# Performance work log

Hardware: AMD Instinct MI355X
Metric: run time of the kernel (lower is better)

## Reference

```python
import jax, jax.numpy as jnp
import numpy as np

NEG = -1e9


def setup_inputs() -> dict:
    key = jax.random.key(0)
    ks = jax.random.split(key, 5)
    B, N, D = 2, 1024, 40
    x = jax.random.normal(ks[0], (B, N, D), dtype=jnp.float32)
    # Linear(2D->D): store as (2D, D) so y = cat @ W1 + b1 (transposed torch layout)
    W1 = jax.random.normal(ks[1], (2 * D, D), dtype=jnp.float32) * (1.0 / np.sqrt(2 * D))
    b1 = jax.random.normal(ks[2], (D,), dtype=jnp.float32) * 0.01
    W2 = jax.random.normal(ks[3], (D, D), dtype=jnp.float32) * (1.0 / np.sqrt(D))
    b2 = jax.random.normal(ks[4], (D,), dtype=jnp.float32) * 0.01
    return {"x": x, "W1": W1, "b1": b1, "W2": W2, "b2": b2}


def reference(x, W1, b1, W2, b2):
    B, N, D = x.shape
    # cat([xi, xj]) @ W1 == xi @ W1[:D] + xj @ W1[D:] -> avoid (B,N,N,2D) materialization
    ai = x @ W1[:D]          # (B, N, D), contribution of row index i
    aj = x @ W1[D:]          # (B, N, D), contribution of col index j
    h = jax.nn.gelu(ai[:, :, None, :] + aj[:, None, :, :] + b1, approximate=False)  # (B,N,N,D)
    p = h @ W2 + b2          # (B, N, N, D)
    mask = jnp.triu(jnp.ones((N, N), dtype=bool), 1)  # True where j > i (masked out)
    p = jnp.where(mask[None, :, :, None], 0.0, p)
    sq = jnp.sum(p * p, axis=-1)                       # (B, N, N)
    s = jnp.sqrt(jnp.where(mask[None], 1.0, sq))       # safe sqrt at masked zeros
    s = jnp.where(mask[None], NEG, s)
    w = jax.nn.softmax(s, axis=-1)                     # softmax over j
    return jnp.sum(w[..., None] * p, axis=2)           # (B, N, D)
```

## Files before the change

### kernel.cpp

```cpp
#include <hip/hip_runtime.h>
#include <math.h>

#define D 40
#define NN 1024
#define BB 2

typedef __attribute__((ext_vector_type(8))) _Float16 f16x8;
typedef __attribute__((ext_vector_type(4))) float f32x4;
typedef __attribute__((ext_vector_type(2))) float f32x2;

__device__ __forceinline__ unsigned int pk16(float a, float b) {
    return __builtin_bit_cast(unsigned int, __builtin_amdgcn_cvt_pkrtz(a, b));
}

__device__ __forceinline__ f32x2 lo2(float4 v) { return (f32x2){v.x, v.y}; }
__device__ __forceinline__ f32x2 hi2(float4 v) { return (f32x2){v.z, v.w}; }

__device__ __forceinline__ unsigned int gelu2pk(f32x2 s) {
    f32x2 u = s * s;
    f32x2 t1 = u * 0.10294366f + 2.3022083f;
    f32x2 z = s * t1;
    f32x2 e = { __builtin_amdgcn_exp2f(z.x), __builtin_amdgcn_exp2f(z.y) };
    e = e + 1.0f;
    f32x2 r = { __builtin_amdgcn_rcpf(e.x), __builtin_amdgcn_rcpf(e.y) };
    f32x2 g = s - s * r;
    return pk16(g.x, g.y);
}

__device__ __forceinline__ void pinf(float& x) { asm volatile("" : "+v"(x)); }
__device__ __forceinline__ void pin4(float4& v) {
    asm volatile("" : "+v"(v.x), "+v"(v.y), "+v"(v.z), "+v"(v.w));
}
__device__ __forceinline__ void pin8(f16x8& v) {
    uint4 u = __builtin_bit_cast(uint4, v);
    asm volatile("" : "+v"(u.x), "+v"(u.y), "+v"(u.z), "+v"(u.w));
    v = __builtin_bit_cast(f16x8, u);
}
__device__ __forceinline__ void pinv4(f32x4& v) {
    asm volatile("" : "+v"(v.x), "+v"(v.y), "+v"(v.z), "+v"(v.w));
}

__device__ __forceinline__ f16x8 frag8(float4 a0, float4 a1, float4 x0, float4 x1) {
    uint4 Bu;
    Bu.x = gelu2pk(lo2(a0) + lo2(x0));
    Bu.y = gelu2pk(hi2(a0) + hi2(x0));
    Bu.z = gelu2pk(lo2(a1) + lo2(x1));
    Bu.w = gelu2pk(hi2(a1) + hi2(x1));
    return __builtin_bit_cast(f16x8, Bu);
}

__global__ __launch_bounds__(256) void precompute_kernel(
    const float* __restrict__ x, const float* __restrict__ W1,
    const float* __restrict__ b1, const float* __restrict__ W2,
    float* __restrict__ ai, float* __restrict__ aj, uint4* __restrict__ w2fT) {
    const int t = threadIdx.x;
    const int bid = blockIdx.x;
    const int r = (bid << 1) + (t >> 7);
    const int tl = t & 127;
    const float* xr = x + (size_t)r * D;

    if (tl < D) {
        const int d = tl;
        float s = b1[d];
#pragma unroll
        for (int k = 0; k < D; ++k) s = fmaf(xr[k], W1[k * D + d], s);
        ai[(size_t)r * D + d] = s;
    } else if (tl >= 64 && tl < 64 + D) {
        const int d = tl - 64;
        float s = 0.0f;
#pragma unroll
        for (int k = 0; k < D; ++k) s = fmaf(xr[k], W1[(D + k) * D + d], s);
        aj[(size_t)r * D + d] = s;
    }

    if (bid == 0 && t < 64) {
        const int lr = t & 15, lg = t >> 4;
#pragma unroll
        for (int mt = 0; mt < 3; ++mt)
#pragma unroll
            for (int kt = 0; kt < 2; ++kt) {
                unsigned int u[4];
#pragma unroll
                for (int pe = 0; pe < 4; ++pe) {
                    int k0 = kt * 32 + lg * 8 + pe * 2;
                    int dd = mt * 16 + lr;
                    float v0 = (k0 < D && dd < D) ? W2[k0 * D + dd] : 0.0f;
                    float v1 = (k0 + 1 < D && dd < D) ? W2[(k0 + 1) * D + dd] : 0.0f;
                    u[pe] = pk16(v0, v1);
                }
                w2fT[(mt * 2 + kt) * 64 + t] = make_uint4(u[0], u[1], u[2], u[3]);
            }
    }
}

__global__ __launch_bounds__(256)
__attribute__((amdgpu_waves_per_eu(4)))
void pair_kernel(
    const float* __restrict__ ai_g, const float* __restrict__ aj_g,
    const uint4* __restrict__ w2fT, const float* __restrict__ b2,
    float* __restrict__ out) {
    __shared__ float mbuf[224];

    const int t = threadIdx.x;
    const int bid = blockIdx.x;
    const int bb = bid & 1;
    const int i = NN - 1 - (bid >> 1);
    const int w = t >> 6;
    const int l = t & 63;
    const int lr = l & 15;
    const int lg = l >> 4;
    const int idxA = lr << 2;

    f16x8 w2t[3][2];
#pragma unroll
    for (int mt = 0; mt < 3; ++mt)
#pragma unroll
        for (int kt = 0; kt < 2; ++kt) {
            w2t[mt][kt] = __builtin_bit_cast(f16x8, w2fT[(mt * 2 + kt) * 64 + l]);
            pin8(w2t[mt][kt]);
        }

    f32x4 bv4[3];
#pragma unroll
    for (int mt = 0; mt < 3; ++mt) {
#pragma unroll
        for (int r = 0; r < 4; ++r) {
            int d = mt * 16 + lg * 4 + r;
            bv4[mt][r] = (d < D) ? b2[d] : 0.0f;
        }
        pinv4(bv4[mt]);
    }

    const float* ai_row = ai_g + ((size_t)bb * NN + i) * D;
    float4 air0 = *reinterpret_cast<const float4*>(ai_row + (lg << 3));
    float4 air1 = *reinterpret_cast<const float4*>(ai_row + (lg << 3) + 4);
    float4 ai32 = *reinterpret_cast<const float4*>(ai_row + 32 + ((l >> 5) << 2));
    pin4(air0); pin4(air1); pin4(ai32);

    const float* aj_b = aj_g + (size_t)bb * NN * D;

    float l_run = 0.0f;
    f32x4 o4[3];
#pragma unroll
    for (int mt = 0; mt < 3; ++mt) o4[mt] = (f32x4){0.0f, 0.0f, 0.0f, 0.0f};

    auto window = [&](int jbase, float4 qa0, float4 qa1, float4 qb0,
                      float4 qb1, float4 qt, bool masked) {
        unsigned int pd0 = gelu2pk(lo2(ai32) + lo2(qt));
        unsigned int pd1 = gelu2pk(hi2(ai32) + hi2(qt));
        uint4 tB0, tB1;
        tB0.x = __builtin_amdgcn_ds_bpermute(idxA,       pd0);
        tB0.y = __builtin_amdgcn_ds_bpermute(idxA,       pd1);
        tB0.z = __builtin_amdgcn_ds_bpermute(idxA + 128, pd0);
        tB0.w = __builtin_amdgcn_ds_bpermute(idxA + 128, pd1);
        tB1.x = __builtin_amdgcn_ds_bpermute(idxA + 64,  pd0);
        tB1.y = __builtin_amdgcn_ds_bpermute(idxA + 64,  pd1);
        tB1.z = __builtin_amdgcn_ds_bpermute(idxA + 192, pd0);
        tB1.w = __builtin_amdgcn_ds_bpermute(idxA + 192, pd1);

        f32x4 acc[3][2];
#pragma unroll
        for (int mt = 0; mt < 3; ++mt)
#pragma unroll
            for (int n = 0; n < 2; ++n)
                acc[mt][n] = bv4[mt];
        {
            f16x8 B = frag8(air0, air1, qa0, qa1);
            f16x8 Bt = __builtin_bit_cast(f16x8, tB0);
#pragma unroll
            for (int mt = 0; mt < 3; ++mt) {
                acc[mt][0] = __builtin_amdgcn_mfma_f32_16x16x32_f16(
                    w2t[mt][0], B, acc[mt][0], 0, 0, 0);
                acc[mt][0] = __builtin_amdgcn_mfma_f32_16x16x32_f16(
                    w2t[mt][1], Bt, acc[mt][0], 0, 0, 0);
            }
        }
        {
            f16x8 B = frag8(air0, air1, qb0, qb1);
            f16x8 Bt = __builtin_bit_cast(f16x8, tB1);
#pragma unroll
            for (int mt = 0; mt < 3; ++mt) {
                acc[mt][1] = __builtin_amdgcn_mfma_f32_16x16x32_f16(
                    w2t[mt][0], B, acc[mt][1], 0, 0, 0);
                acc[mt][1] = __builtin_amdgcn_mfma_f32_16x16x32_f16(
                    w2t[mt][1], Bt, acc[mt][1], 0, 0, 0);
            }
        }

        float sv[2];
#pragma unroll
        for (int n = 0; n < 2; ++n) {
            f32x4 sq4 = acc[0][n] * acc[0][n];
            sq4 = acc[1][n] * acc[1][n] + sq4;
            sq4 = acc[2][n] * acc[2][n] + sq4;
            float sq = (sq4.x + sq4.y) + (sq4.z + sq4.w);
            sq += __shfl_xor(sq, 16);
            sq += __shfl_xor(sq, 32);
            if (masked) {
                int j = jbase + n * 16 + lr;
                sv[n] = (j <= i) ? __builtin_amdgcn_sqrtf(sq) : -1e30f;
            } else {
                sv[n] = __builtin_amdgcn_sqrtf(sq);
            }
        }
        float w0 = __expf(sv[0]);
        float w1 = __expf(sv[1]);
        l_run += w0 + w1;
#pragma unroll
        for (int mt = 0; mt < 3; ++mt) {
            o4[mt] = acc[mt][1] * w1 + o4[mt];
            o4[mt] = acc[mt][0] * w0 + o4[mt];
        }
    };

    int jbase = w << 5;
    const float* pA = aj_b + (size_t)(jbase + lr) * D + (lg << 3);
    const float* pT = aj_b + (size_t)(jbase + (l & 31)) * D + 32 + ((l >> 5) << 2);
    for (; jbase + 31 <= i; jbase += 128) {
        float4 qa0 = *reinterpret_cast<const float4*>(pA);
        float4 qa1 = *reinterpret_cast<const float4*>(pA + 4);
        float4 qb0 = *reinterpret_cast<const float4*>(pA + 16 * D);
        float4 qb1 = *reinterpret_cast<const float4*>(pA + 16 * D + 4);
        float4 qt  = *reinterpret_cast<const float4*>(pT);
        pA += 128 * D;
        pT += 128 * D;
        window(jbase, qa0, qa1, qb0, qb1, qt, false);
    }
    if (jbase <= i) {
        const int j0 = min(jbase + lr, i);
        const int j1 = min(jbase + 16 + lr, i);
        const int jt = min(jbase + (l & 31), i);
        const float* r0 = aj_b + (size_t)j0 * D + (lg << 3);
        const float* r1 = aj_b + (size_t)j1 * D + (lg << 3);
        float4 qa0 = *reinterpret_cast<const float4*>(r0);
        float4 qa1 = *reinterpret_cast<const float4*>(r0 + 4);
        float4 qb0 = *reinterpret_cast<const float4*>(r1);
        float4 qb1 = *reinterpret_cast<const float4*>(r1 + 4);
        float4 qt  = *reinterpret_cast<const float4*>(
            aj_b + (size_t)jt * D + 32 + ((l >> 5) << 2));
        window(jbase, qa0, qa1, qb0, qb1, qt, true);
    }

#pragma unroll
    for (int mt = 0; mt < 3; ++mt)
#pragma unroll
        for (int r = 0; r < 4; ++r) {
            float v = o4[mt][r];
            v += __shfl_xor(v, 1);
            v += __shfl_xor(v, 2);
            v += __shfl_xor(v, 4);
            v += __shfl_xor(v, 8);
            o4[mt][r] = v;
        }
    l_run += __shfl_xor(l_run, 1);
    l_run += __shfl_xor(l_run, 2);
    l_run += __shfl_xor(l_run, 4);
    l_run += __shfl_xor(l_run, 8);

    if (lr == 0) {
#pragma unroll
        for (int mt = 0; mt < 3; ++mt)
#pragma unroll
            for (int r = 0; r < 4; ++r) {
                int d = mt * 16 + lg * 4 + r;
                if (d < D) mbuf[w * 56 + d] = o4[mt][r];
            }
        if (lg == 0) mbuf[w * 56 + 48] = l_run;
    }
    __syncthreads();
    if (t < D) {
        float L = mbuf[48] + mbuf[56 + 48] + mbuf[112 + 48] + mbuf[168 + 48];
        float val = mbuf[t] + mbuf[56 + t] + mbuf[112 + t] + mbuf[168 + t];
        out[((size_t)bb * NN + i) * D + t] = val / L;
    }
}

extern "C" void kernel_launch(void* const* d_in, const int* in_sizes, int n_in,
                              void* d_out, int out_size, void* d_ws, size_t ws_size,
                              hipStream_t stream) {
    const float* x  = (const float*)d_in[0];
    const float* W1 = (const float*)d_in[1];
    const float* b1 = (const float*)d_in[2];
    const float* W2 = (const float*)d_in[3];
    const float* b2 = (const float*)d_in[4];
    float* out = (float*)d_out;

    float* ai = (float*)d_ws;
    float* aj = ai + (size_t)BB * NN * D;
    uint4* w2fT = (uint4*)(aj + (size_t)BB * NN * D);

    precompute_kernel<<<BB * NN / 2, 256, 0, stream>>>(x, W1, b1, W2, ai, aj, w2fT);
    pair_kernel<<<BB * NN, 256, 0, stream>>>(ai, aj, w2fT, b2, out);
}
```

Measured before the change: 31.79 us.

## Pair complementary rows per block for balanced triangular work and fold b2 into MFMA

Each 512-thread block now handles row i = N-1-p together with row p, so every block covers exactly 33 windows of 32 columns and the triangular workload is balanced across blocks. The 8 waves walk a combined window index, flushing partial sums into a per-row shared slot whenever they switch rows. The b2 bias is packed into the padded k=40 row of the W2 fragment, and a constant 1.0 is injected into the matching activation lane, so the bias is added inside the MFMA and no longer needs bias registers. The cost is larger blocks, a row-switch branch inside the loop, and an extra reduction pass over 8 waves.

```diff
diff --git a/kernel.cpp b/kernel.cpp
--- a/kernel.cpp
+++ b/kernel.cpp
@@ -27,7 +27,6 @@
     return pk16(g.x, g.y);
 }
 
-__device__ __forceinline__ void pinf(float& x) { asm volatile("" : "+v"(x)); }
 __device__ __forceinline__ void pin4(float4& v) {
     asm volatile("" : "+v"(v.x), "+v"(v.y), "+v"(v.z), "+v"(v.w));
 }
@@ -35,9 +34,6 @@
     uint4 u = __builtin_bit_cast(uint4, v);
     asm volatile("" : "+v"(u.x), "+v"(u.y), "+v"(u.z), "+v"(u.w));
     v = __builtin_bit_cast(f16x8, u);
-}
-__device__ __forceinline__ void pinv4(f32x4& v) {
-    asm volatile("" : "+v"(v.x), "+v"(v.y), "+v"(v.z), "+v"(v.w));
 }
 
 __device__ __forceinline__ f16x8 frag8(float4 a0, float4 a1, float4 x0, float4 x1) {
@@ -52,6 +48,7 @@
 __global__ __launch_bounds__(256) void precompute_kernel(
     const float* __restrict__ x, const float* __restrict__ W1,
     const float* __restrict__ b1, const float* __restrict__ W2,
+    const float* __restrict__ b2,
     float* __restrict__ ai, float* __restrict__ aj, uint4* __restrict__ w2fT) {
     const int t = threadIdx.x;
     const int bid = blockIdx.x;
@@ -84,8 +81,12 @@
                 for (int pe = 0; pe < 4; ++pe) {
                     int k0 = kt * 32 + lg * 8 + pe * 2;
                     int dd = mt * 16 + lr;
-                    float v0 = (k0 < D && dd < D) ? W2[k0 * D + dd] : 0.0f;
-                    float v1 = (k0 + 1 < D && dd < D) ? W2[(k0 + 1) * D + dd] : 0.0f;
+                    float v0 = 0.0f, v1 = 0.0f;
+                    if (dd < D) {
+                        if (k0 < D) v0 = W2[k0 * D + dd];
+                        else if (k0 == D) v0 = b2[dd];
+                        if (k0 + 1 < D) v1 = W2[(k0 + 1) * D + dd];
+                    }
                     u[pe] = pk16(v0, v1);
                 }
                 w2fT[(mt * 2 + kt) * 64 + t] = make_uint4(u[0], u[1], u[2], u[3]);
@@ -93,24 +94,27 @@
     }
 }
 
-__global__ __launch_bounds__(256)
-__attribute__((amdgpu_waves_per_eu(4)))
+__global__ __launch_bounds__(512)
+__attribute__((amdgpu_waves_per_eu(6)))
 void pair_kernel(
     const float* __restrict__ ai_g, const float* __restrict__ aj_g,
-    const uint4* __restrict__ w2fT, const float* __restrict__ b2,
-    float* __restrict__ out) {
-    __shared__ float mbuf[224];
+    const uint4* __restrict__ w2fT, float* __restrict__ out) {
+    __shared__ float mbuf[2 * 8 * 44];
 
     const int t = threadIdx.x;
     const int bid = blockIdx.x;
     const int bb = bid & 1;
-    const int i = NN - 1 - (bid >> 1);
-    const int w = t >> 6;
+    const int p = bid >> 1;
+    const int hi = NN - 1 - p;
+    const int lo = p;
+    const int W = t >> 6;
     const int l = t & 63;
     const int lr = l & 15;
     const int lg = l >> 4;
     const int idxA = lr << 2;
 
+    for (int k = t; k < 2 * 8 * 44; k += 512) mbuf[k] = 0.0f;
+
     f16x8 w2t[3][2];
 #pragma unroll
     for (int mt = 0; mt < 3; ++mt)
@@ -120,29 +124,51 @@
             pin8(w2t[mt][kt]);
         }
 
-    f32x4 bv4[3];
-#pragma unroll
-    for (int mt = 0; mt < 3; ++mt) {
-#pragma unroll
-        for (int r = 0; r < 4; ++r) {
-            int d = mt * 16 + lg * 4 + r;
-            bv4[mt][r] = (d < D) ? b2[d] : 0.0f;
-        }
-        pinv4(bv4[mt]);
-    }
-
-    const float* ai_row = ai_g + ((size_t)bb * NN + i) * D;
+    const int Whi = ((NN - p) + 31) >> 5;
+    const float* aj_b = aj_g + (size_t)bb * NN * D;
+
+    int cur_i = hi;
+    const float* ai_row = ai_g + ((size_t)bb * NN + hi) * D;
     float4 air0 = *reinterpret_cast<const float4*>(ai_row + (lg << 3));
     float4 air1 = *reinterpret_cast<const float4*>(ai_row + (lg << 3) + 4);
     float4 ai32 = *reinterpret_cast<const float4*>(ai_row + 32 + ((l >> 5) << 2));
     pin4(air0); pin4(air1); pin4(ai32);
 
-    const float* aj_b = aj_g + (size_t)bb * NN * D;
-
     float l_run = 0.0f;
     f32x4 o4[3];
 #pragma unroll
     for (int mt = 0; mt < 3; ++mt) o4[mt] = (f32x4){0.0f, 0.0f, 0.0f, 0.0f};
+
+    __syncthreads();
+
+    auto flush = [&](int slot) {
+#pragma unroll
+        for (int mt = 0; mt < 3; ++mt)
+#pragma unroll
+            for (int r = 0; r < 4; ++r) {
+                float v = o4[mt][r];
+                v += __shfl_xor(v, 1);
+                v += __shfl_xor(v, 2);
+                v += __shfl_xor(v, 4);
+                v += __shfl_xor(v, 8);
+                o4[mt][r] = v;
+            }
+        l_run += __shfl_xor(l_run, 1);
+        l_run += __shfl_xor(l_run, 2);
+        l_run += __shfl_xor(l_run, 4);
+        l_run += __shfl_xor(l_run, 8);
+        if (lr == 0) {
+            float* mb = mbuf + slot * 8 * 44 + W * 44;
+#pragma unroll
+            for (int mt = 0; mt < 3; ++mt)
+#pragma unroll
+                for (int r = 0; r < 4; ++r) {
+                    int d = mt * 16 + lg * 4 + r;
+                    if (d < D) mb[d] = o4[mt][r];
+                }
+            if (lg == 0) mb[40] = l_run;
+        }
+    };
 
     auto window = [&](int jbase, float4 qa0, float4 qa1, float4 qb0,
                       float4 qb1, float4 qt, bool masked) {
@@ -157,13 +183,17 @@
         tB1.y = __builtin_amdgcn_ds_bpermute(idxA + 64,  pd1);
         tB1.z = __builtin_amdgcn_ds_bpermute(idxA + 192, pd0);
         tB1.w = __builtin_amdgcn_ds_bpermute(idxA + 192, pd1);
+        if (lg == 1) {
+            tB0.x = (tB0.x & 0xffff0000u) | 0x3C00u;
+            tB1.x = (tB1.x & 0xffff0000u) | 0x3C00u;
+        }
 
         f32x4 acc[3][2];
 #pragma unroll
         for (int mt = 0; mt < 3; ++mt)
 #pragma unroll
             for (int n = 0; n < 2; ++n)
-                acc[mt][n] = bv4[mt];
+                acc[mt][n] = (f32x4){0.0f, 0.0f, 0.0f, 0.0f};
         {
             f16x8 B = frag8(air0, air1, qa0, qa1);
             f16x8 Bt = __builtin_bit_cast(f16x8, tB0);
@@ -198,7 +228,7 @@
             sq += __shfl_xor(sq, 32);
             if (masked) {
                 int j = jbase + n * 16 + lr;
-                sv[n] = (j <= i) ? __builtin_amdgcn_sqrtf(sq) : -1e30f;
+                sv[n] = (j <= cur_i) ? __builtin_amdgcn_sqrtf(sq) : -1e30f;
             } else {
                 sv[n] = __builtin_amdgcn_sqrtf(sq);
             }
@@ -213,65 +243,63 @@
         }
     };
 
-    int jbase = w << 5;
-    const float* pA = aj_b + (size_t)(jbase + lr) * D + (lg << 3);
-    const float* pT = aj_b + (size_t)(jbase + (l & 31)) * D + 32 + ((l >> 5) << 2);
-    for (; jbase + 31 <= i; jbase += 128) {
-        float4 qa0 = *reinterpret_cast<const float4*>(pA);
-        float4 qa1 = *reinterpret_cast<const float4*>(pA + 4);
-        float4 qb0 = *reinterpret_cast<const float4*>(pA + 16 * D);
-        float4 qb1 = *reinterpret_cast<const float4*>(pA + 16 * D + 4);
-        float4 qt  = *reinterpret_cast<const float4*>(pT);
-        pA += 128 * D;
-        pT += 128 * D;
-        window(jbase, qa0, qa1, qb0, qb1, qt, false);
+    for (int g = W; g < 33; g += 8) {
+        const bool is_hi = (g < Whi);
+        if (!is_hi && cur_i != lo) {
+            flush(0);
+            l_run = 0.0f;
+#pragma unroll
+            for (int mt = 0; mt < 3; ++mt) o4[mt] = (f32x4){0.0f, 0.0f, 0.0f, 0.0f};
+            cur_i = lo;
+            ai_row = ai_g + ((size_t)bb * NN + lo) * D;
+            air0 = *reinterpret_cast<const float4*>(ai_row + (lg << 3));
+            air1 = *reinterpret_cast<const float4*>(ai_row + (lg << 3) + 4);
+            ai32 = *reinterpret_cast<const float4*>(ai_row + 32 + ((l >> 5) << 2));
+            pin4(air0); pin4(air1); pin4(ai32);
+        }
+        const int jbase = (is_hi ? g : g - Whi) << 5;
+        const bool masked = (jbase + 31 > cur_i);
+        float4 qa0, qa1, qb0, qb1, qt;
+        if (!masked) {
+            const float* r0 = aj_b + (size_t)(jbase + lr) * D + (lg << 3);
+            qa0 = *reinterpret_cast<const float4*>(r0);
+            qa1 = *reinterpret_cast<const float4*>(r0 + 4);
+            qb0 = *reinterpret_cast<const float4*>(r0 + 16 * D);
+            qb1 = *reinterpret_cast<const float4*>(r0 + 16 * D + 4);
+            qt  = *reinterpret_cast<const float4*>(
+                aj_b + (size_t)(jbase + (l & 31)) * D + 32 + ((l >> 5) << 2));
+        } else {
+            const int j0 = min(jbase + lr, cur_i);
+            const int j1 = min(jbase + 16 + lr, cur_i);
+            const int jt = min(jbase + (l & 31), cur_i);
+            const float* r0 = aj_b + (size_t)j0 * D + (lg << 3);
+            const float* r1 = aj_b + (size_t)j1 * D + (lg << 3);
+            qa0 = *reinterpret_cast<const float4*>(r0);
+            qa1 = *reinterpret_cast<const float4*>(r0 + 4);
+            qb0 = *reinterpret_cast<const float4*>(r1);
+            qb1 = *reinterpret_cast<const float4*>(r1 + 4);
+            qt  = *reinterpret_cast<const float4*>(
+                aj_b + (size_t)jt * D + 32 + ((l >> 5) << 2));
+        }
+        window(jbase, qa0, qa1, qb0, qb1, qt, masked);
     }
-    if (jbase <= i) {
-        const int j0 = min(jbase + lr, i);
-        const int j1 = min(jbase + 16 + lr, i);
-        const int jt = min(jbase + (l & 31), i);
-        const float* r0 = aj_b + (size_t)j0 * D + (lg << 3);
-        const float* r1 = aj_b + (size_t)j1 * D + (lg << 3);
-        float4 qa0 = *reinterpret_cast<const float4*>(r0);
-        float4 qa1 = *reinterpret_cast<const float4*>(r0 + 4);
-        float4 qb0 = *reinterpret_cast<const float4*>(r1);
-        float4 qb1 = *reinterpret_cast<const float4*>(r1 + 4);
-        float4 qt  = *reinterpret_cast<const float4*>(
-            aj_b + (size_t)jt * D + 32 + ((l >> 5) << 2));
-        window(jbase, qa0, qa1, qb0, qb1, qt, true);
-    }
-
-#pragma unroll
-    for (int mt = 0; mt < 3; ++mt)
-#pragma unroll
-        for (int r = 0; r < 4; ++r) {
-            float v = o4[mt][r];
-            v += __shfl_xor(v, 1);
-            v += __shfl_xor(v, 2);
-            v += __shfl_xor(v, 4);
-            v += __shfl_xor(v, 8);
-            o4[mt][r] = v;
-        }
-    l_run += __shfl_xor(l_run, 1);
-    l_run += __shfl_xor(l_run, 2);
-    l_run += __shfl_xor(l_run, 4);
-    l_run += __shfl_xor(l_run, 8);
-
-    if (lr == 0) {
-#pragma unroll
-        for (int mt = 0; mt < 3; ++mt)
-#pragma unroll
-            for (int r = 0; r < 4; ++r) {
-                int d = mt * 16 + lg * 4 + r;
-                if (d < D) mbuf[w * 56 + d] = o4[mt][r];
-            }
-        if (lg == 0) mbuf[w * 56 + 48] = l_run;
-    }
+    flush(cur_i == lo ? 1 : 0);
     __syncthreads();
+
     if (t < D) {
-        float L = mbuf[48] + mbuf[56 + 48] + mbuf[112 + 48] + mbuf[168 + 48];
-        float val = mbuf[t] + mbuf[56 + t] + mbuf[112 + t] + mbuf[168 + t];
-        out[((size_t)bb * NN + i) * D + t] = val / L;
+        float val = 0.0f, L = 0.0f;
+#pragma unroll
+        for (int q = 0; q < 8; ++q) { val += mbuf[q * 44 + t]; L += mbuf[q * 44 + 40]; }
+        out[((size_t)bb * NN + hi) * D + t] = val / L;
+    } else if (t >= 64 && t < 64 + D) {
+        const int d = t - 64;
+        float val = 0.0f, L = 0.0f;
+#pragma unroll
+        for (int q = 0; q < 8; ++q) {
+            val += mbuf[8 * 44 + q * 44 + d];
+            L += mbuf[8 * 44 + q * 44 + 40];
+        }
+        out[((size_t)bb * NN + lo) * D + d] = val / L;
     }
 }
 
@@ -289,6 +317,6 @@
     float* aj = ai + (size_t)BB * NN * D;
     uint4* w2fT = (uint4*)(aj + (size_t)BB * NN * D);
 
-    precompute_kernel<<<BB * NN / 2, 256, 0, stream>>>(x, W1, b1, W2, ai, aj, w2fT);
-    pair_kernel<<<BB * NN, 256, 0, stream>>>(ai, aj, w2fT, b2, out);
-}
+    precompute_kernel<<<BB * NN / 2, 256, 0, stream>>>(x, W1, b1, W2, b2, ai, aj, w2fT);
+    pair_kernel<<<BB * NN / 2, 512, 0, stream>>>(ai, aj, w2fT, out);
+}
```

Result: slower. 118.6 us (+273.2%).
